# Kernel tuning notes

Measured on AMD Instinct MI355X. Metric: run time of the kernel, lower is better.

## Reference

```python
import jax, jax.numpy as jnp
import numpy as np

B, L, C = 8, 8192, 256
FOCAL_LEVEL = 3
KERNELS = [3, 5, 7]  # focal_factor*k + focal_x[0]
LN_EPS = 1e-3  # keras LayerNormalization default epsilon


def _gelu(x):
    return jax.nn.gelu(x, approximate=False)  # keras 'gelu' is exact


def _layernorm(x, g, b):
    m = jnp.mean(x, axis=-1, keepdims=True)
    v = jnp.var(x, axis=-1, keepdims=True)
    return (x - m) * jax.lax.rsqrt(v + LN_EPS) * g + b


def _conv1d_same(x, w, b):
    # x: [B,L,Cin], w: [K,Cin,Cout]
    y = jax.lax.conv_general_dilated(x, w, window_strides=(1,), padding='SAME',
                                     dimension_numbers=('NWC', 'WIO', 'NWC'))
    return y + b


def setup_inputs() -> dict:
    key = jax.random.key(0)
    ks = jax.random.split(key, 16)
    s = 0.02
    inp = {
        'x': jax.random.normal(ks[0], (B, L, C), dtype=jnp.float32),
        'f_w': jax.random.normal(ks[1], (C, 2 * C + FOCAL_LEVEL + 1), dtype=jnp.float32) * s,
        'f_b': jnp.zeros((2 * C + FOCAL_LEVEL + 1,), dtype=jnp.float32),
        'h_w': jax.random.normal(ks[2], (1, C, C), dtype=jnp.float32) * s,
        'h_b': jnp.zeros((C,), dtype=jnp.float32),
        'proj_w': jax.random.normal(ks[3], (C, C), dtype=jnp.float32) * s,
        'proj_b': jnp.zeros((C,), dtype=jnp.float32),
    }
    for l, K in enumerate(KERNELS):
        inp[f'conv_w{l}'] = jax.random.normal(ks[4 + l], (K, C, C), dtype=jnp.float32) * s
        inp[f'conv_b{l}'] = jnp.zeros((C,), dtype=jnp.float32)
        inp[f'ln_g{l}'] = jnp.ones((C,), dtype=jnp.float32)
        inp[f'ln_b{l}'] = jnp.zeros((C,), dtype=jnp.float32)
    return inp


def reference(x, f_w, f_b,
              conv_w0, conv_b0, ln_g0, ln_b0,
              conv_w1, conv_b1, ln_g1, ln_b1,
              conv_w2, conv_b2, ln_g2, ln_b2,
              h_w, h_b, proj_w, proj_b):
    x_fea = x @ f_w + f_b                      # [B,L,2C+4]
    q = x_fea[..., :C]
    ctx = x_fea[..., C:2 * C]
    gates = x_fea[..., 2 * C:]                 # [B,L,4]

    levels = [(conv_w0, conv_b0, ln_g0, ln_b0),
              (conv_w1, conv_b1, ln_g1, ln_b1),
              (conv_w2, conv_b2, ln_g2, ln_b2)]

    ctx_all = jnp.zeros_like(ctx)
    for l, (cw, cb, lg, lb) in enumerate(levels):
        ctx = _layernorm(_gelu(_conv1d_same(ctx, cw, cb)), lg, lb)
        ctx_all = ctx_all + ctx * gates[..., l:l + 1]

    # global average pool gate (broadcasts over L)
    ctx_global = jnp.mean(ctx, axis=1, keepdims=True) * gates[..., FOCAL_LEVEL:]
    ctx_all = ctx_all + ctx_global

    # h: 1x1 conv == dense
    ctx_all = jnp.einsum('blc,cd->bld', ctx_all, h_w[0]) + h_b
    x_out = (q * ctx_all) @ proj_w + proj_b    # proj_drop is identity at inference
    return x_out
```

## Files before the change

### kernel.cpp

```cpp
#include <hip/hip_runtime.h>
#include <math.h>

#define CDIM 256
#define LSEQ 8192
#define BATCH 8
#define MTOT (BATCH * LSEQ)
#define PADROWS 8208
#define PAD0 8

typedef unsigned short ushort_t;
typedef unsigned int uint_t;

typedef __bf16 bf16x8 __attribute__((ext_vector_type(8)));
typedef float f32x4 __attribute__((ext_vector_type(4)));

__device__ __forceinline__ ushort_t f2bf(float f) {
    union { float f; uint_t u; } v; v.f = f;
    uint_t u = v.u;
    return (ushort_t)((u + 0x7FFFu + ((u >> 16) & 1u)) >> 16);
}
__device__ __forceinline__ float bf2f(ushort_t h) {
    union { uint_t u; float f; } v; v.u = ((uint_t)h) << 16;
    return v.f;
}
__device__ __forceinline__ float gelu_exact(float x) {
    return 0.5f * x * (1.0f + erff(x * 0.70710678118654752440f));
}

__device__ __forceinline__ void gload16(const ushort_t* g, ushort_t* lds) {
    __builtin_amdgcn_global_load_lds(
        reinterpret_cast<__attribute__((address_space(1))) uint_t*>(
            reinterpret_cast<uintptr_t>(g)),
        reinterpret_cast<__attribute__((address_space(3))) uint_t*>(
            reinterpret_cast<uintptr_t>(lds)),
        16, 0, 0);
}

__global__ __launch_bounds__(256) void cvt_gates(
    const float* __restrict__ x, const float* __restrict__ f_w,
    const float* __restrict__ f_b,
    ushort_t* __restrict__ x_bf, float* __restrict__ gates)
{
    __shared__ float fcol[256][4];
    int tid = threadIdx.x;
    #pragma unroll
    for (int j = 0; j < 4; ++j) fcol[tid][j] = f_w[(size_t)tid * 516 + 512 + j];
    __syncthreads();
    int w = tid >> 6, l = tid & 63;
    size_t t = (size_t)blockIdx.x * 4 + w;
    float4 xv = ((const float4*)(x + t * CDIM))[l];
    ((ushort4*)(x_bf + t * CDIM))[l] =
        make_ushort4(f2bf(xv.x), f2bf(xv.y), f2bf(xv.z), f2bf(xv.w));
    int c = l * 4;
    float a[4];
    #pragma unroll
    for (int j = 0; j < 4; ++j)
        a[j] = xv.x * fcol[c][j] + xv.y * fcol[c + 1][j] + xv.z * fcol[c + 2][j] + xv.w * fcol[c + 3][j];
    #pragma unroll
    for (int off = 32; off >= 1; off >>= 1)
        #pragma unroll
        for (int j = 0; j < 4; ++j) a[j] += __shfl_xor(a[j], off);
    if (l == 0) {
        #pragma unroll
        for (int j = 0; j < 4; ++j) gates[t * 4 + j] = a[j] + f_b[512 + j];
    }
}

__global__ __launch_bounds__(256) void prep_weights(
    const float* __restrict__ f_w,  const float* __restrict__ c0,
    const float* __restrict__ c1,   const float* __restrict__ c2,
    const float* __restrict__ h_w,  const float* __restrict__ p_w,
    ushort_t* __restrict__ f_wT, ushort_t* __restrict__ c0T,
    ushort_t* __restrict__ c1T,  ushort_t* __restrict__ c2T,
    ushort_t* __restrict__ h_wT, ushort_t* __restrict__ p_wT)
{
    __shared__ float t[32][33];
    int r = blockIdx.x;
    const float* in; ushort_t* out; int Kt, ldin;
    if (r < 128)              { in = f_w; out = f_wT; Kt = 8;  ldin = 516; }
    else if ((r -= 128) < 192){ in = c0;  out = c0T;  Kt = 24; ldin = 256; }
    else if ((r -= 192) < 320){ in = c1;  out = c1T;  Kt = 40; ldin = 256; }
    else if ((r -= 320) < 448){ in = c2;  out = c2T;  Kt = 56; ldin = 256; }
    else if ((r -= 448) < 64) { in = h_w; out = h_wT; Kt = 8;  ldin = 256; }
    else                      { r -= 64; in = p_w; out = p_wT; Kt = 8; ldin = 256; }
    int K = Kt * 32;
    int k0 = (r % Kt) * 32, n0 = (r / Kt) * 32;
    int tx = threadIdx.x & 31, ty = threadIdx.x >> 5;
    #pragma unroll
    for (int i = 0; i < 4; i++) {
        int k = k0 + ty + i * 8;
        t[ty + i * 8][tx] = in[(size_t)k * ldin + n0 + tx];
    }
    __syncthreads();
    #pragma unroll
    for (int i = 0; i < 4; i++) {
        int n = n0 + ty + i * 8;
        out[(size_t)n * K + k0 + tx] = f2bf(t[tx][ty + i * 8]);
    }
}

__global__ __launch_bounds__(256) void zero_guards_all(ushort_t* __restrict__ ctx_base) {
    int i = blockIdx.x * 256 + threadIdx.x;
    int buf = i >> 15;
    int j = i & 32767;
    int c = j & 255;
    int rr = (j >> 8) & 15;
    int b = j >> 12;
    size_t row = (size_t)b * PADROWS + ((rr < 8) ? rr : (PADROWS - 16 + rr));
    ctx_base[((size_t)buf * BATCH * PADROWS + row) * CDIM + c] = 0;
}

template <int MODE>
__global__ __launch_bounds__(256) void gemm_bf16(
    const ushort_t* __restrict__ A, const ushort_t* __restrict__ BT,
    const float* __restrict__ bias,
    float* __restrict__ C, ushort_t* __restrict__ q_out, ushort_t* __restrict__ ctx_pad,
    int Ktot)
{
    __shared__ __align__(16) ushort_t As[128 * 32];
    __shared__ __align__(16) ushort_t Bs[128 * 32];
    int tid = threadIdx.x;
    int w = tid >> 6, l = tid & 63;

    int hw = blockIdx.x + gridDim.x * blockIdx.y;
    int N = gridDim.x * gridDim.y;
    int tile = (hw & 7) * (N >> 3) + (hw >> 3);
    int bx = tile % gridDim.x;
    int by = tile / gridDim.x;

    int bn = bx * 128;
    long arow0 = (long)by * 128;
    int crow0 = by * 128;

    int wr = w >> 1, wc = w & 1;
    int lr = l & 15, lk = (l >> 4) * 8;
    int sr = l >> 2;
    int sc = (l & 3) * 8;

    f32x4 acc[4][4] = {};

    int nsteps = Ktot >> 5;
    for (int kt = 0; kt < nsteps; ++kt) {
        int k0 = kt << 5;
        #pragma unroll
        for (int jj = 0; jj < 2; ++jj) {
            int j = w * 2 + jj;
            int r = j * 16 + sr;
            gload16(A + (arow0 + r) * CDIM + (k0 + sc), &As[j * 512]);
            gload16(BT + (long)(bn + r) * Ktot + (k0 + sc), &Bs[j * 512]);
        }
        __syncthreads();
        bf16x8 av[4], bv[4];
        #pragma unroll
        for (int m = 0; m < 4; ++m)
            av[m] = *reinterpret_cast<const bf16x8*>(&As[(wr * 64 + m * 16 + lr) * 32 + lk]);
        #pragma unroll
        for (int n = 0; n < 4; ++n)
            bv[n] = *reinterpret_cast<const bf16x8*>(&Bs[(wc * 64 + n * 16 + lr) * 32 + lk]);
        #pragma unroll
        for (int m = 0; m < 4; ++m)
            #pragma unroll
            for (int n = 0; n < 4; ++n)
                acc[m][n] = __builtin_amdgcn_mfma_f32_16x16x32_bf16(av[m], bv[n], acc[m][n], 0, 0, 0);
        __syncthreads();
    }

    int rbase = (l >> 4) * 4;
    #pragma unroll
    for (int n = 0; n < 4; ++n) {
        int col = bn + wc * 64 + n * 16 + lr;
        float bia = bias[col];
        #pragma unroll
        for (int m = 0; m < 4; ++m) {
            int rowb = crow0 + wr * 64 + m * 16 + rbase;
            #pragma unroll
            for (int r = 0; r < 4; ++r) {
                float v = acc[m][n][r] + bia;
                int row = rowb + r;
                if (MODE == 0) {
                    C[(size_t)row * CDIM + col] = v;
                } else if (MODE == 1) {
                    if (col < CDIM) {
                        q_out[(size_t)row * CDIM + col] = f2bf(v);
                    } else {
                        int bb = row >> 13, tb = row & (LSEQ - 1);
                        ctx_pad[((size_t)bb * PADROWS + PAD0 + tb) * CDIM + (col - CDIM)] = f2bf(v);
                    }
                } else {
                    size_t idx = (size_t)row * CDIM + col;
                    q_out[idx] = f2bf(bf2f(q_out[idx]) * v);
                }
            }
        }
    }
}

__device__ __forceinline__ void stageA128(const ushort_t* Arow0, int cc,
                                          ushort_t* asb, int tid, int w) {
    int row = tid >> 2, cp = tid & 3;
    int cg = cp ^ ((row >> 1) & 3);
    gload16(Arow0 + (size_t)row * CDIM + cc * 32 + cg * 8, asb + (size_t)(w * 64) * 8);
    if (tid < 64) {
        int o2 = 512 + tid;
        int row2 = o2 >> 2, cp2 = o2 & 3;
        int cg2 = cp2 ^ ((row2 >> 1) & 3);
        gload16(Arow0 + (size_t)row2 * CDIM + cc * 32 + cg2 * 8, asb + (size_t)512 * 8);
    }
}
__device__ __forceinline__ void stageB128(const ushort_t* BT, int Ktot, int koffB,
                                          ushort_t* bsb, int tid) {
    #pragma unroll
    for (int i = 0; i < 2; ++i) {
        int o = tid + i * 512;
        int n = o >> 2, cp = o & 3;
        int cg = cp ^ ((n >> 1) & 3);
        gload16(BT + (size_t)n * Ktot + koffB + cg * 8,
                bsb + (size_t)((o >> 6) * 64) * 8);
    }
}

__global__ __launch_bounds__(512, 4) void conv_fused(
    const ushort_t* __restrict__ A, const ushort_t* __restrict__ BT,
    const float* __restrict__ bias,
    const float* __restrict__ lng, const float* __restrict__ lnb,
    ushort_t* __restrict__ ctx_out, int KW, int Ktot)
{
    __shared__ __align__(16) ushort_t As2[2][144 * 32];
    __shared__ __align__(16) ushort_t Bs[2][256 * 32];

    int tid = threadIdx.x;
    int w = tid >> 6, l = tid & 63;
    int by = blockIdx.x;
    int b = by >> 6;
    int tloc = (by & 63) << 7;
    const ushort_t* Arow0 = A + ((size_t)b * PADROWS + PAD0 + tloc - 8) * CDIM;

    int wr = w >> 2;
    int wc = w & 3;
    int lr = l & 15;
    int quad = l >> 4;

    int P = KW >> 1;
    int hoff = 8 - P;
    f32x4 acc[4][4] = {};

    stageA128(Arow0, 0, As2[0], tid, w);
    stageB128(BT, Ktot, 0, Bs[0], tid);
    __syncthreads();

    int nIt = KW * 8;
    int it = 0;
    for (int c = 0; c < 8; ++c) {
        for (int tap = 0; tap < KW; ++tap, ++it) {
            if (tap == 0 && c < 7)
                stageA128(Arow0, c + 1, As2[(c + 1) & 1], tid, w);
            if (it + 1 < nIt) {
                int tapn = tap + 1, cn = c;
                if (tapn == KW) { tapn = 0; cn = c + 1; }
                stageB128(BT, Ktot, tapn * 256 + cn * 32, Bs[(it + 1) & 1], tid);
            }
            const ushort_t* asb = As2[c & 1];
            const ushort_t* bsb = Bs[it & 1];
            bf16x8 av[4], bv[4];
            #pragma unroll
            for (int m = 0; m < 4; ++m) {
                int row = wr * 64 + m * 16 + lr + tap + hoff;
                int cs = quad ^ ((row >> 1) & 3);
                av[m] = *reinterpret_cast<const bf16x8*>(&asb[row * 32 + cs * 8]);
            }
            #pragma unroll
            for (int n = 0; n < 4; ++n) {
                int nn = wc * 64 + n * 16 + lr;
                int cs = quad ^ ((nn >> 1) & 3);
                bv[n] = *reinterpret_cast<const bf16x8*>(&bsb[nn * 32 + cs * 8]);
            }
            #pragma unroll
            for (int m = 0; m < 4; ++m)
                #pragma unroll
                for (int n = 0; n < 4; ++n)
                    acc[m][n] = __builtin_amdgcn_mfma_f32_16x16x32_bf16(av[m], bv[n], acc[m][n], 0, 0, 0);
            __syncthreads();
        }
    }

    float* rs = (float*)&Bs[0][0];
    float* rq = rs + 512;
    float bias_c[4], lng_c[4], lnb_c[4];
    #pragma unroll
    for (int n = 0; n < 4; ++n) {
        int col = wc * 64 + n * 16 + lr;
        bias_c[n] = bias[col];
        lng_c[n] = lng[col];
        lnb_c[n] = lnb[col];
    }
    #pragma unroll
    for (int m = 0; m < 4; ++m) {
        #pragma unroll
        for (int r = 0; r < 4; ++r) {
            float s = 0.0f, sq = 0.0f;
            #pragma unroll
            for (int n = 0; n < 4; ++n) {
                float v = acc[m][n][r] + bias_c[n];
                v = gelu_exact(v);
                acc[m][n][r] = v;
                s += v; sq += v * v;
            }
            s += __shfl_xor(s, 1);  sq += __shfl_xor(sq, 1);
            s += __shfl_xor(s, 2);  sq += __shfl_xor(sq, 2);
            s += __shfl_xor(s, 4);  sq += __shfl_xor(sq, 4);
            s += __shfl_xor(s, 8);  sq += __shfl_xor(sq, 8);
            if (lr == 0) {
                int rl = wr * 64 + m * 16 + quad * 4 + r;
                rs[rl * 4 + wc] = s;
                rq[rl * 4 + wc] = sq;
            }
        }
    }
    __syncthreads();
    #pragma unroll
    for (int m = 0; m < 4; ++m) {
        #pragma unroll
        for (int r = 0; r < 4; ++r) {
            int rl = wr * 64 + m * 16 + quad * 4 + r;
            float mean = (rs[rl * 4] + rs[rl * 4 + 1] + rs[rl * 4 + 2] + rs[rl * 4 + 3]) * (1.0f / 256.0f);
            float var = (rq[rl * 4] + rq[rl * 4 + 1] + rq[rl * 4 + 2] + rq[rl * 4 + 3]) * (1.0f / 256.0f) - mean * mean;
            float inv = rsqrtf(var + 1e-3f);
            int trow = tloc + rl;
            ushort_t* cp = ctx_out + ((size_t)b * PADROWS + PAD0 + trow) * CDIM;
            #pragma unroll
            for (int n = 0; n < 4; ++n) {
                int col = wc * 64 + n * 16 + lr;
                float y = (acc[m][n][r] - mean) * inv * lng_c[n] + lnb_c[n];
                cp[col] = f2bf(y);
            }
        }
    }
}

__global__ __launch_bounds__(256) void col_mean_partial(const ushort_t* __restrict__ ctx_pad,
                                                        float* __restrict__ partial) {
    int b = blockIdx.x, chunk = blockIdx.y, c = threadIdx.x;
    const ushort_t* base = ctx_pad + ((size_t)b * PADROWS + PAD0 + chunk * 256) * CDIM + c;
    float s = 0.0f;
    for (int r = 0; r < 256; ++r) s += bf2f(base[(size_t)r * CDIM]);
    partial[((size_t)b * 32 + chunk) * CDIM + c] = s;
}

__global__ __launch_bounds__(256) void col_mean_final(const float* __restrict__ partial,
                                                      float* __restrict__ meanv) {
    int b = blockIdx.x, c = threadIdx.x;
    float s = 0.0f;
    for (int i = 0; i < 32; ++i) s += partial[((size_t)b * 32 + i) * CDIM + c];
    meanv[b * CDIM + c] = s * (1.0f / (float)LSEQ);
}

__global__ __launch_bounds__(256) void finalize_A(
    const ushort_t* __restrict__ c0buf, const ushort_t* __restrict__ c1buf,
    const ushort_t* __restrict__ c2buf,
    const float* __restrict__ meanv, const float* __restrict__ gates,
    ushort_t* __restrict__ A_bf)
{
    int i = blockIdx.x * 256 + threadIdx.x;
    int t = i >> 5;
    int c8 = (i & 31) * 8;
    int b = t >> 13, tb = t & (LSEQ - 1);
    size_t pidx = ((size_t)b * PADROWS + PAD0 + tb) * CDIM + c8;
    const float* g = gates + (size_t)t * 4;
    float g0 = g[0], g1 = g[1], g2 = g[2], g3 = g[3];
    ushort4 a0 = *(const ushort4*)(c0buf + pidx);
    ushort4 a1 = *(const ushort4*)(c0buf + pidx + 4);
    ushort4 b0 = *(const ushort4*)(c1buf + pidx);
    ushort4 b1 = *(const ushort4*)(c1buf + pidx + 4);
    ushort4 d0 = *(const ushort4*)(c2buf + pidx);
    ushort4 d1 = *(const ushort4*)(c2buf + pidx + 4);
    const float* mv = meanv + b * CDIM + c8;
    ushort_t out[8];
    ushort_t va[8] = { a0.x, a0.y, a0.z, a0.w, a1.x, a1.y, a1.z, a1.w };
    ushort_t vb[8] = { b0.x, b0.y, b0.z, b0.w, b1.x, b1.y, b1.z, b1.w };
    ushort_t vd[8] = { d0.x, d0.y, d0.z, d0.w, d1.x, d1.y, d1.z, d1.w };
    #pragma unroll
    for (int j = 0; j < 8; ++j) {
        float v = bf2f(va[j]) * g0 + bf2f(vb[j]) * g1 + bf2f(vd[j]) * g2 + mv[j] * g3;
        out[j] = f2bf(v);
    }
    *(ushort4*)(A_bf + (size_t)t * CDIM + c8)     = make_ushort4(out[0], out[1], out[2], out[3]);
    *(ushort4*)(A_bf + (size_t)t * CDIM + c8 + 4) = make_ushort4(out[4], out[5], out[6], out[7]);
}

extern "C" void kernel_launch(void* const* d_in, const int* in_sizes, int n_in,
                              void* d_out, int out_size, void* d_ws, size_t ws_size,
                              hipStream_t stream) {
    const float* x      = (const float*)d_in[0];
    const float* f_w    = (const float*)d_in[1];
    const float* f_b    = (const float*)d_in[2];
    const float* h_w    = (const float*)d_in[3];
    const float* h_b    = (const float*)d_in[4];
    const float* proj_w = (const float*)d_in[5];
    const float* proj_b = (const float*)d_in[6];
    const float* conv_w[3] = { (const float*)d_in[7],  (const float*)d_in[11], (const float*)d_in[15] };
    const float* conv_b[3] = { (const float*)d_in[8],  (const float*)d_in[12], (const float*)d_in[16] };
    const float* ln_g[3]   = { (const float*)d_in[9],  (const float*)d_in[13], (const float*)d_in[17] };
    const float* ln_b[3]   = { (const float*)d_in[10], (const float*)d_in[14], (const float*)d_in[18] };

    const size_t MC = (size_t)MTOT * CDIM;
    const size_t PADC = (size_t)BATCH * PADROWS * CDIM;
    char* w = (char*)d_ws;
    ushort_t* x_bf  = (ushort_t*)w;  w += MC * 2;
    ushort_t* q_bf  = (ushort_t*)w;  w += MC * 2;
    ushort_t* ctxF  = (ushort_t*)w;  w += PADC * 2;
    ushort_t* ctx0  = (ushort_t*)w;  w += PADC * 2;
    ushort_t* ctx1  = (ushort_t*)w;  w += PADC * 2;
    ushort_t* ctx2  = (ushort_t*)w;  w += PADC * 2;
    float* gates    = (float*)w;     w += (size_t)MTOT * 4 * 4;
    float* partial  = (float*)w;     w += (size_t)8 * 32 * CDIM * 4;
    float* meanv    = (float*)w;     w += (size_t)8 * CDIM * 4;
    ushort_t* f_wT  = (ushort_t*)w;  w += (size_t)512 * 256 * 2;
    ushort_t* convT0 = (ushort_t*)w; w += (size_t)768 * 256 * 2;
    ushort_t* convT1 = (ushort_t*)w; w += (size_t)1280 * 256 * 2;
    ushort_t* convT2 = (ushort_t*)w; w += (size_t)1792 * 256 * 2;
    ushort_t* h_wT   = (ushort_t*)w; w += (size_t)256 * 256 * 2;
    ushort_t* proj_wT = (ushort_t*)w; w += (size_t)256 * 256 * 2;
    ushort_t* A_bf = x_bf;

    dim3 blk(256);

    cvt_gates<<<dim3(MTOT / 4), blk, 0, stream>>>(x, f_w, f_b, x_bf, gates);
    prep_weights<<<dim3(1216), blk, 0, stream>>>(f_w, conv_w[0], conv_w[1], conv_w[2],
        h_w, proj_w, f_wT, convT0, convT1, convT2, h_wT, proj_wT);
    zero_guards_all<<<dim3(512), blk, 0, stream>>>(ctxF);

    gemm_bf16<1><<<dim3(4, 512), blk, 0, stream>>>(x_bf, f_wT, f_b,
        nullptr, q_bf, ctxF, 256);

    conv_fused<<<dim3(512), dim3(512), 0, stream>>>(ctxF, convT0, conv_b[0],
        ln_g[0], ln_b[0], ctx0, 3, 768);
    conv_fused<<<dim3(512), dim3(512), 0, stream>>>(ctx0, convT1, conv_b[1],
        ln_g[1], ln_b[1], ctx1, 5, 1280);
    conv_fused<<<dim3(512), dim3(512), 0, stream>>>(ctx1, convT2, conv_b[2],
        ln_g[2], ln_b[2], ctx2, 7, 1792);

    col_mean_partial<<<dim3(BATCH, 32), blk, 0, stream>>>(ctx2, partial);
    col_mean_final<<<dim3(BATCH), blk, 0, stream>>>(partial, meanv);

    finalize_A<<<dim3(MTOT * 32 / 256), blk, 0, stream>>>(ctx0, ctx1, ctx2,
        meanv, gates, A_bf);

    gemm_bf16<2><<<dim3(2, 512), blk, 0, stream>>>(A_bf, h_wT, h_b,
        nullptr, q_bf, nullptr, 256);
    gemm_bf16<0><<<dim3(2, 512), blk, 0, stream>>>(q_bf, proj_wT, proj_b,
        (float*)d_out, nullptr, nullptr, 256);
}
```

Measured before the change: 360.1 us.

## Fuse gated context sum and column mean into last conv epilogue

The last conv level's epilogue now computes the gated sum of the three context levels and writes it directly. It also accumulates per-block column sums for the global mean. The global-pool term is pushed through the h projection algebraically (mean @ h_w computed once per batch) and added in the h-GEMM epilogue. This removes the ctx2 buffer, the separate column-mean kernels and the finalize kernel, along with their full-tensor reads and writes, at the cost of extra loads in the conv epilogue and LDS atomics.

```diff
diff --git a/kernel.cpp b/kernel.cpp
--- a/kernel.cpp
+++ b/kernel.cpp
@@ -115,6 +115,7 @@
     const ushort_t* __restrict__ A, const ushort_t* __restrict__ BT,
     const float* __restrict__ bias,
     float* __restrict__ C, ushort_t* __restrict__ q_out, ushort_t* __restrict__ ctx_pad,
+    const float* __restrict__ gates, const float* __restrict__ hmean,
     int Ktot)
 {
     __shared__ __align__(16) ushort_t As[128 * 32];
@@ -175,11 +176,11 @@
             int rowb = crow0 + wr * 64 + m * 16 + rbase;
             #pragma unroll
             for (int r = 0; r < 4; ++r) {
-                float v = acc[m][n][r] + bia;
                 int row = rowb + r;
                 if (MODE == 0) {
-                    C[(size_t)row * CDIM + col] = v;
+                    C[(size_t)row * CDIM + col] = acc[m][n][r] + bia;
                 } else if (MODE == 1) {
+                    float v = acc[m][n][r] + bia;
                     if (col < CDIM) {
                         q_out[(size_t)row * CDIM + col] = f2bf(v);
                     } else {
@@ -187,6 +188,8 @@
                         ctx_pad[((size_t)bb * PADROWS + PAD0 + tb) * CDIM + (col - CDIM)] = f2bf(v);
                     }
                 } else {
+                    float g3 = gates[(size_t)row * 4 + 3];
+                    float v = acc[m][n][r] + bia + g3 * hmean[(row >> 13) * CDIM + col];
                     size_t idx = (size_t)row * CDIM + col;
                     q_out[idx] = f2bf(bf2f(q_out[idx]) * v);
                 }
@@ -219,11 +222,15 @@
     }
 }
 
+template <int FUSE>
 __global__ __launch_bounds__(512, 4) void conv_fused(
     const ushort_t* __restrict__ A, const ushort_t* __restrict__ BT,
     const float* __restrict__ bias,
     const float* __restrict__ lng, const float* __restrict__ lnb,
-    ushort_t* __restrict__ ctx_out, int KW, int Ktot)
+    ushort_t* __restrict__ ctx_out, int KW, int Ktot,
+    const ushort_t* __restrict__ c0in, const ushort_t* __restrict__ c1in,
+    const float* __restrict__ gates,
+    ushort_t* __restrict__ ctxS, float* __restrict__ colpart)
 {
     __shared__ __align__(16) ushort_t As2[2][144 * 32];
     __shared__ __align__(16) ushort_t Bs[2][256 * 32];
@@ -285,6 +292,7 @@
 
     float* rs = (float*)&Bs[0][0];
     float* rq = rs + 512;
+    float* colsum = rs + 1024;
     float bias_c[4], lng_c[4], lnb_c[4];
     #pragma unroll
     for (int n = 0; n < 4; ++n) {
@@ -293,6 +301,7 @@
         lng_c[n] = lng[col];
         lnb_c[n] = lnb[col];
     }
+    if (FUSE && tid < 256) colsum[tid] = 0.0f;
     #pragma unroll
     for (int m = 0; m < 4; ++m) {
         #pragma unroll
@@ -317,6 +326,8 @@
         }
     }
     __syncthreads();
+
+    float colacc[4] = {0.0f, 0.0f, 0.0f, 0.0f};
     #pragma unroll
     for (int m = 0; m < 4; ++m) {
         #pragma unroll
@@ -326,65 +337,52 @@
             float var = (rq[rl * 4] + rq[rl * 4 + 1] + rq[rl * 4 + 2] + rq[rl * 4 + 3]) * (1.0f / 256.0f) - mean * mean;
             float inv = rsqrtf(var + 1e-3f);
             int trow = tloc + rl;
-            ushort_t* cp = ctx_out + ((size_t)b * PADROWS + PAD0 + trow) * CDIM;
-            #pragma unroll
-            for (int n = 0; n < 4; ++n) {
-                int col = wc * 64 + n * 16 + lr;
-                float y = (acc[m][n][r] - mean) * inv * lng_c[n] + lnb_c[n];
-                cp[col] = f2bf(y);
+            long grow = (long)by * 128 + rl;
+            if (!FUSE) {
+                ushort_t* cp = ctx_out + ((size_t)b * PADROWS + PAD0 + trow) * CDIM;
+                #pragma unroll
+                for (int n = 0; n < 4; ++n) {
+                    int col = wc * 64 + n * 16 + lr;
+                    float y = (acc[m][n][r] - mean) * inv * lng_c[n] + lnb_c[n];
+                    cp[col] = f2bf(y);
+                }
+            } else {
+                size_t prow = ((size_t)b * PADROWS + PAD0 + trow) * CDIM;
+                float4 gv = *(const float4*)(gates + grow * 4);
+                ushort_t* sp = ctxS + (size_t)grow * CDIM;
+                #pragma unroll
+                for (int n = 0; n < 4; ++n) {
+                    int col = wc * 64 + n * 16 + lr;
+                    float y = (acc[m][n][r] - mean) * inv * lng_c[n] + lnb_c[n];
+                    colacc[n] += y;
+                    float sv = gv.x * bf2f(c0in[prow + col]) + gv.y * bf2f(c1in[prow + col]) + gv.z * y;
+                    sp[col] = f2bf(sv);
+                }
             }
         }
     }
-}
-
-__global__ __launch_bounds__(256) void col_mean_partial(const ushort_t* __restrict__ ctx_pad,
-                                                        float* __restrict__ partial) {
-    int b = blockIdx.x, chunk = blockIdx.y, c = threadIdx.x;
-    const ushort_t* base = ctx_pad + ((size_t)b * PADROWS + PAD0 + chunk * 256) * CDIM + c;
-    float s = 0.0f;
-    for (int r = 0; r < 256; ++r) s += bf2f(base[(size_t)r * CDIM]);
-    partial[((size_t)b * 32 + chunk) * CDIM + c] = s;
-}
-
-__global__ __launch_bounds__(256) void col_mean_final(const float* __restrict__ partial,
-                                                      float* __restrict__ meanv) {
+    if (FUSE) {
+        #pragma unroll
+        for (int n = 0; n < 4; ++n)
+            atomicAdd(&colsum[wc * 64 + n * 16 + lr], colacc[n]);
+        __syncthreads();
+        if (tid < 256) colpart[(size_t)by * 256 + tid] = colsum[tid];
+    }
+}
+
+__global__ __launch_bounds__(256) void mean_hmean(
+    const float* __restrict__ colpart, const float* __restrict__ h_w,
+    float* __restrict__ hmean)
+{
+    __shared__ float mv[256];
     int b = blockIdx.x, c = threadIdx.x;
     float s = 0.0f;
-    for (int i = 0; i < 32; ++i) s += partial[((size_t)b * 32 + i) * CDIM + c];
-    meanv[b * CDIM + c] = s * (1.0f / (float)LSEQ);
-}
-
-__global__ __launch_bounds__(256) void finalize_A(
-    const ushort_t* __restrict__ c0buf, const ushort_t* __restrict__ c1buf,
-    const ushort_t* __restrict__ c2buf,
-    const float* __restrict__ meanv, const float* __restrict__ gates,
-    ushort_t* __restrict__ A_bf)
-{
-    int i = blockIdx.x * 256 + threadIdx.x;
-    int t = i >> 5;
-    int c8 = (i & 31) * 8;
-    int b = t >> 13, tb = t & (LSEQ - 1);
-    size_t pidx = ((size_t)b * PADROWS + PAD0 + tb) * CDIM + c8;
-    const float* g = gates + (size_t)t * 4;
-    float g0 = g[0], g1 = g[1], g2 = g[2], g3 = g[3];
-    ushort4 a0 = *(const ushort4*)(c0buf + pidx);
-    ushort4 a1 = *(const ushort4*)(c0buf + pidx + 4);
-    ushort4 b0 = *(const ushort4*)(c1buf + pidx);
-    ushort4 b1 = *(const ushort4*)(c1buf + pidx + 4);
-    ushort4 d0 = *(const ushort4*)(c2buf + pidx);
-    ushort4 d1 = *(const ushort4*)(c2buf + pidx + 4);
-    const float* mv = meanv + b * CDIM + c8;
-    ushort_t out[8];
-    ushort_t va[8] = { a0.x, a0.y, a0.z, a0.w, a1.x, a1.y, a1.z, a1.w };
-    ushort_t vb[8] = { b0.x, b0.y, b0.z, b0.w, b1.x, b1.y, b1.z, b1.w };
-    ushort_t vd[8] = { d0.x, d0.y, d0.z, d0.w, d1.x, d1.y, d1.z, d1.w };
-    #pragma unroll
-    for (int j = 0; j < 8; ++j) {
-        float v = bf2f(va[j]) * g0 + bf2f(vb[j]) * g1 + bf2f(vd[j]) * g2 + mv[j] * g3;
-        out[j] = f2bf(v);
-    }
-    *(ushort4*)(A_bf + (size_t)t * CDIM + c8)     = make_ushort4(out[0], out[1], out[2], out[3]);
-    *(ushort4*)(A_bf + (size_t)t * CDIM + c8 + 4) = make_ushort4(out[4], out[5], out[6], out[7]);
+    for (int t = 0; t < 64; ++t) s += colpart[((size_t)(b * 64 + t)) * 256 + c];
+    mv[c] = s * (1.0f / (float)LSEQ);
+    __syncthreads();
+    float acc = 0.0f;
+    for (int k = 0; k < 256; ++k) acc += mv[k] * h_w[(size_t)k * 256 + c];
+    hmean[b * 256 + c] = acc;
 }
 
 extern "C" void kernel_launch(void* const* d_in, const int* in_sizes, int n_in,
@@ -410,43 +408,38 @@
     ushort_t* ctxF  = (ushort_t*)w;  w += PADC * 2;
     ushort_t* ctx0  = (ushort_t*)w;  w += PADC * 2;
     ushort_t* ctx1  = (ushort_t*)w;  w += PADC * 2;
-    ushort_t* ctx2  = (ushort_t*)w;  w += PADC * 2;
+    ushort_t* ctxS  = (ushort_t*)w;  w += MC * 2;
     float* gates    = (float*)w;     w += (size_t)MTOT * 4 * 4;
-    float* partial  = (float*)w;     w += (size_t)8 * 32 * CDIM * 4;
-    float* meanv    = (float*)w;     w += (size_t)8 * CDIM * 4;
+    float* colpart  = (float*)w;     w += (size_t)512 * 256 * 4;
+    float* hmean    = (float*)w;     w += (size_t)8 * 256 * 4;
     ushort_t* f_wT  = (ushort_t*)w;  w += (size_t)512 * 256 * 2;
     ushort_t* convT0 = (ushort_t*)w; w += (size_t)768 * 256 * 2;
     ushort_t* convT1 = (ushort_t*)w; w += (size_t)1280 * 256 * 2;
     ushort_t* convT2 = (ushort_t*)w; w += (size_t)1792 * 256 * 2;
     ushort_t* h_wT   = (ushort_t*)w; w += (size_t)256 * 256 * 2;
     ushort_t* proj_wT = (ushort_t*)w; w += (size_t)256 * 256 * 2;
-    ushort_t* A_bf = x_bf;
 
     dim3 blk(256);
 
     cvt_gates<<<dim3(MTOT / 4), blk, 0, stream>>>(x, f_w, f_b, x_bf, gates);
     prep_weights<<<dim3(1216), blk, 0, stream>>>(f_w, conv_w[0], conv_w[1], conv_w[2],
         h_w, proj_w, f_wT, convT0, convT1, convT2, h_wT, proj_wT);
-    zero_guards_all<<<dim3(512), blk, 0, stream>>>(ctxF);
+    zero_guards_all<<<dim3(384), blk, 0, stream>>>(ctxF);
 
     gemm_bf16<1><<<dim3(4, 512), blk, 0, stream>>>(x_bf, f_wT, f_b,
-        nullptr, q_bf, ctxF, 256);
-
-    conv_fused<<<dim3(512), dim3(512), 0, stream>>>(ctxF, convT0, conv_b[0],
-        ln_g[0], ln_b[0], ctx0, 3, 768);
-    conv_fused<<<dim3(512), dim3(512), 0, stream>>>(ctx0, convT1, conv_b[1],
-        ln_g[1], ln_b[1], ctx1, 5, 1280);
-    conv_fused<<<dim3(512), dim3(512), 0, stream>>>(ctx1, convT2, conv_b[2],
-        ln_g[2], ln_b[2], ctx2, 7, 1792);
-
-    col_mean_partial<<<dim3(BATCH, 32), blk, 0, stream>>>(ctx2, partial);
-    col_mean_final<<<dim3(BATCH), blk, 0, stream>>>(partial, meanv);
-
-    finalize_A<<<dim3(MTOT * 32 / 256), blk, 0, stream>>>(ctx0, ctx1, ctx2,
-        meanv, gates, A_bf);
-
-    gemm_bf16<2><<<dim3(2, 512), blk, 0, stream>>>(A_bf, h_wT, h_b,
-        nullptr, q_bf, nullptr, 256);
+        nullptr, q_bf, ctxF, nullptr, nullptr, 256);
+
+    conv_fused<0><<<dim3(512), dim3(512), 0, stream>>>(ctxF, convT0, conv_b[0],
+        ln_g[0], ln_b[0], ctx0, 3, 768, nullptr, nullptr, nullptr, nullptr, nullptr);
+    conv_fused<0><<<dim3(512), dim3(512), 0, stream>>>(ctx0, convT1, conv_b[1],
+        ln_g[1], ln_b[1], ctx1, 5, 1280, nullptr, nullptr, nullptr, nullptr, nullptr);
+    conv_fused<1><<<dim3(512), dim3(512), 0, stream>>>(ctx1, convT2, conv_b[2],
+        ln_g[2], ln_b[2], nullptr, 7, 1792, ctx0, ctx1, gates, ctxS, colpart);
+
+    mean_hmean<<<dim3(BATCH), blk, 0, stream>>>(colpart, h_w, hmean);
+
+    gemm_bf16<3><<<dim3(2, 512), blk, 0, stream>>>(ctxS, h_wT, h_b,
+        nullptr, q_bf, nullptr, gates, hmean, 256);
     gemm_bf16<0><<<dim3(2, 512), blk, 0, stream>>>(q_bf, proj_wT, proj_b,
-        (float*)d_out, nullptr, nullptr, 256);
-}
+        (float*)d_out, nullptr, nullptr, nullptr, nullptr, 256);
+}
```

Result: slower. 491.9 us (+36.6%).

## Load conv weights directly from global memory and template conv kernel on kernel width

Applied to the files above, without the earlier changes.

The conv_fused kernel no longer stages the weight (B) tiles through double-buffered LDS. Each lane now reads its bf16x8 weight fragments straight from global memory, so the per-tap __syncthreads is removed and only one barrier per channel chunk remains. The kernel is templated on KW so the tap loop fully unrolls and Ktot and the padding offset become compile-time constants. This drops LDS traffic and barrier stalls, but relies on L2/L1 caching of weights shared across all blocks and may expose global load latency in front of the MFMAs.

```diff
diff --git a/kernel.cpp b/kernel.cpp
--- a/kernel.cpp
+++ b/kernel.cpp
@@ -207,26 +207,17 @@
         gload16(Arow0 + (size_t)row2 * CDIM + cc * 32 + cg2 * 8, asb + (size_t)512 * 8);
     }
 }
-__device__ __forceinline__ void stageB128(const ushort_t* BT, int Ktot, int koffB,
-                                          ushort_t* bsb, int tid) {
-    #pragma unroll
-    for (int i = 0; i < 2; ++i) {
-        int o = tid + i * 512;
-        int n = o >> 2, cp = o & 3;
-        int cg = cp ^ ((n >> 1) & 3);
-        gload16(BT + (size_t)n * Ktot + koffB + cg * 8,
-                bsb + (size_t)((o >> 6) * 64) * 8);
-    }
-}
-
+
+template <int KW>
 __global__ __launch_bounds__(512, 4) void conv_fused(
     const ushort_t* __restrict__ A, const ushort_t* __restrict__ BT,
     const float* __restrict__ bias,
     const float* __restrict__ lng, const float* __restrict__ lnb,
-    ushort_t* __restrict__ ctx_out, int KW, int Ktot)
+    ushort_t* __restrict__ ctx_out)
 {
+    constexpr int Ktot = KW * 256;
     __shared__ __align__(16) ushort_t As2[2][144 * 32];
-    __shared__ __align__(16) ushort_t Bs[2][256 * 32];
+    __shared__ float rs[128][4], rq[128][4];
 
     int tid = threadIdx.x;
     int w = tid >> 6, l = tid & 63;
@@ -240,28 +231,30 @@
     int lr = l & 15;
     int quad = l >> 4;
 
-    int P = KW >> 1;
-    int hoff = 8 - P;
+    constexpr int P = KW >> 1;
+    constexpr int hoff = 8 - P;
     f32x4 acc[4][4] = {};
 
+    const ushort_t* Bbase[4];
+    #pragma unroll
+    for (int n = 0; n < 4; ++n) {
+        int nn = wc * 64 + n * 16 + lr;
+        Bbase[n] = BT + (size_t)nn * Ktot + quad * 8;
+    }
+
     stageA128(Arow0, 0, As2[0], tid, w);
-    stageB128(BT, Ktot, 0, Bs[0], tid);
     __syncthreads();
 
-    int nIt = KW * 8;
-    int it = 0;
     for (int c = 0; c < 8; ++c) {
-        for (int tap = 0; tap < KW; ++tap, ++it) {
-            if (tap == 0 && c < 7)
-                stageA128(Arow0, c + 1, As2[(c + 1) & 1], tid, w);
-            if (it + 1 < nIt) {
-                int tapn = tap + 1, cn = c;
-                if (tapn == KW) { tapn = 0; cn = c + 1; }
-                stageB128(BT, Ktot, tapn * 256 + cn * 32, Bs[(it + 1) & 1], tid);
-            }
-            const ushort_t* asb = As2[c & 1];
-            const ushort_t* bsb = Bs[it & 1];
+        if (c < 7)
+            stageA128(Arow0, c + 1, As2[(c + 1) & 1], tid, w);
+        const ushort_t* asb = As2[c & 1];
+        #pragma unroll
+        for (int tap = 0; tap < KW; ++tap) {
             bf16x8 av[4], bv[4];
+            #pragma unroll
+            for (int n = 0; n < 4; ++n)
+                bv[n] = *reinterpret_cast<const bf16x8*>(Bbase[n] + tap * 256 + c * 32);
             #pragma unroll
             for (int m = 0; m < 4; ++m) {
                 int row = wr * 64 + m * 16 + lr + tap + hoff;
@@ -269,22 +262,14 @@
                 av[m] = *reinterpret_cast<const bf16x8*>(&asb[row * 32 + cs * 8]);
             }
             #pragma unroll
-            for (int n = 0; n < 4; ++n) {
-                int nn = wc * 64 + n * 16 + lr;
-                int cs = quad ^ ((nn >> 1) & 3);
-                bv[n] = *reinterpret_cast<const bf16x8*>(&bsb[nn * 32 + cs * 8]);
-            }
-            #pragma unroll
             for (int m = 0; m < 4; ++m)
                 #pragma unroll
                 for (int n = 0; n < 4; ++n)
                     acc[m][n] = __builtin_amdgcn_mfma_f32_16x16x32_bf16(av[m], bv[n], acc[m][n], 0, 0, 0);
-            __syncthreads();
         }
-    }
-
-    float* rs = (float*)&Bs[0][0];
-    float* rq = rs + 512;
+        __syncthreads();
+    }
+
     float bias_c[4], lng_c[4], lnb_c[4];
     #pragma unroll
     for (int n = 0; n < 4; ++n) {
@@ -311,8 +296,8 @@
             s += __shfl_xor(s, 8);  sq += __shfl_xor(sq, 8);
             if (lr == 0) {
                 int rl = wr * 64 + m * 16 + quad * 4 + r;
-                rs[rl * 4 + wc] = s;
-                rq[rl * 4 + wc] = sq;
+                rs[rl][wc] = s;
+                rq[rl][wc] = sq;
             }
         }
     }
@@ -322,8 +307,8 @@
         #pragma unroll
         for (int r = 0; r < 4; ++r) {
             int rl = wr * 64 + m * 16 + quad * 4 + r;
-            float mean = (rs[rl * 4] + rs[rl * 4 + 1] + rs[rl * 4 + 2] + rs[rl * 4 + 3]) * (1.0f / 256.0f);
-            float var = (rq[rl * 4] + rq[rl * 4 + 1] + rq[rl * 4 + 2] + rq[rl * 4 + 3]) * (1.0f / 256.0f) - mean * mean;
+            float mean = (rs[rl][0] + rs[rl][1] + rs[rl][2] + rs[rl][3]) * (1.0f / 256.0f);
+            float var = (rq[rl][0] + rq[rl][1] + rq[rl][2] + rq[rl][3]) * (1.0f / 256.0f) - mean * mean;
             float inv = rsqrtf(var + 1e-3f);
             int trow = tloc + rl;
             ushort_t* cp = ctx_out + ((size_t)b * PADROWS + PAD0 + trow) * CDIM;
@@ -432,12 +417,12 @@
     gemm_bf16<1><<<dim3(4, 512), blk, 0, stream>>>(x_bf, f_wT, f_b,
         nullptr, q_bf, ctxF, 256);
 
-    conv_fused<<<dim3(512), dim3(512), 0, stream>>>(ctxF, convT0, conv_b[0],
-        ln_g[0], ln_b[0], ctx0, 3, 768);
-    conv_fused<<<dim3(512), dim3(512), 0, stream>>>(ctx0, convT1, conv_b[1],
-        ln_g[1], ln_b[1], ctx1, 5, 1280);
-    conv_fused<<<dim3(512), dim3(512), 0, stream>>>(ctx1, convT2, conv_b[2],
-        ln_g[2], ln_b[2], ctx2, 7, 1792);
+    conv_fused<3><<<dim3(512), dim3(512), 0, stream>>>(ctxF, convT0, conv_b[0],
+        ln_g[0], ln_b[0], ctx0);
+    conv_fused<5><<<dim3(512), dim3(512), 0, stream>>>(ctx0, convT1, conv_b[1],
+        ln_g[1], ln_b[1], ctx1);
+    conv_fused<7><<<dim3(512), dim3(512), 0, stream>>>(ctx1, convT2, conv_b[2],
+        ln_g[2], ln_b[2], ctx2);
 
     col_mean_partial<<<dim3(BATCH, 32), blk, 0, stream>>>(ctx2, partial);
     col_mean_final<<<dim3(BATCH), blk, 0, stream>>>(partial, meanv);
```

Measured after the change: 608.9 us. 69.1% more time.
